# Kernel optimization log

Hardware: AMD Instinct MI355X
Metric: run time of the kernel (lower is better)

The kernel has to match this reference:

```python
import jax, jax.numpy as jnp
import numpy as np

N_NODES = 100000
HIDDEN = 128
N_EDGES = 1000000


def setup_inputs() -> dict:
    key = jax.random.key(0)
    k1, k2, k3 = jax.random.split(key, 3)
    z = jax.random.normal(k1, (N_NODES, HIDDEN), dtype=jnp.float32)
    edge_index = jax.random.randint(k2, (2, N_EDGES), 0, N_NODES, dtype=jnp.int64)
    # xavier_uniform for square matrix: bound = sqrt(6/(fan_in+fan_out))
    bound = float(np.sqrt(6.0 / (HIDDEN + HIDDEN)))
    weights = jax.random.uniform(k3, (HIDDEN, HIDDEN), dtype=jnp.float32,
                                 minval=-bound, maxval=bound)
    return {"z": z, "edge_index": edge_index, "weights": weights}


def reference(z, edge_index, weights):
    # symm=True: symmetrize the bilinear form
    W = weights + weights.T                      # [d, d]
    z_src = z[edge_index[0]]                     # [E, d] gather
    z_dst = z[edge_index[1]]                     # [E, d] gather
    # torch: (W @ z_dst.T).T == z_dst @ W.T
    value = jnp.einsum('ed,dk,ek->e', z_src, W, z_dst)  # row-wise bilinear score
    return jax.nn.sigmoid(value)
```

## Files before the change

### kernel.cpp

```cpp
#include <hip/hip_runtime.h>

#define HIDDEN 128
#define LDSW 130

typedef _Float16 f16;
typedef f16 f16x2 __attribute__((ext_vector_type(2)));
typedef f16 f16x4 __attribute__((ext_vector_type(4)));

static __device__ __forceinline__ float fdot2(f16x2 a, f16x2 b, float c) {
    return __builtin_amdgcn_fdot2(a, b, c, false);
}

__global__ __launch_bounds__(256) void prep_w(const float* __restrict__ w,
                                              f16* __restrict__ wsh_t) {
    int idx = blockIdx.x * 256 + threadIdx.x;
    int j = idx >> 7, k = idx & 127;
    wsh_t[idx] = (f16)(w[k * HIDDEN + j] + w[j * HIDDEN + k]);
}

__global__ __launch_bounds__(256) void gemm_u16(const float* __restrict__ z,
                                               const f16* __restrict__ wsh_t,
                                               f16* __restrict__ zh,
                                               f16* __restrict__ uh) {
    __shared__ f16 wlt[HIDDEN * LDSW];
    __shared__ f16 zt[32 * HIDDEN];
    int tid = threadIdx.x;

    {
        const float4* g = (const float4*)wsh_t;
        #pragma unroll
        for (int it = 0; it < 8; ++it) {
            int idx = it * 256 + tid;
            float4 v = g[idx];
            int j = idx >> 4, kc = idx & 15;
            f16x2* dst = (f16x2*)&wlt[j * LDSW + kc * 8];
            const f16x2* s = (const f16x2*)&v;
            dst[0] = s[0]; dst[1] = s[1]; dst[2] = s[2]; dst[3] = s[3];
        }
    }
    int row0 = blockIdx.x * 32;
    {
        const float4* z4 = (const float4*)(z + (size_t)row0 * HIDDEN);
        f16x2* zl = (f16x2*)zt;
        f16x2* zg = (f16x2*)(zh + (size_t)row0 * HIDDEN);
        #pragma unroll
        for (int it = 0; it < 4; ++it) {
            int idx = it * 256 + tid;
            float4 v = z4[idx];
            f16x2 h0 = {(f16)v.x, (f16)v.y};
            f16x2 h1 = {(f16)v.z, (f16)v.w};
            int r = idx >> 5, c4 = idx & 31;
            zl[r * 64 + c4 * 2]     = h0;
            zl[r * 64 + c4 * 2 + 1] = h1;
            zg[idx * 2]     = h0;
            zg[idx * 2 + 1] = h1;
        }
    }
    __syncthreads();

    int wave = tid >> 6, lane = tid & 63;
    float acc0[8], acc1[8];
    #pragma unroll
    for (int r = 0; r < 8; ++r) { acc0[r] = 0.f; acc1[r] = 0.f; }

    const f16x2* wl2 = (const f16x2*)wlt;
    int c0 = lane * 65, c1 = (lane + 64) * 65;

    #pragma unroll 4
    for (int q = 0; q < 32; ++q) {
        f16x2 w00 = wl2[c0 + 2 * q], w01 = wl2[c0 + 2 * q + 1];
        f16x2 w10 = wl2[c1 + 2 * q], w11 = wl2[c1 + 2 * q + 1];
        #pragma unroll
        for (int r = 0; r < 8; ++r) {
            f16x4 zv = *(const f16x4*)&zt[(wave * 8 + r) * HIDDEN + 4 * q];
            f16x2 z0 = {zv.x, zv.y}, z1 = {zv.z, zv.w};
            acc0[r] = fdot2(z1, w01, fdot2(z0, w00, acc0[r]));
            acc1[r] = fdot2(z1, w11, fdot2(z0, w10, acc1[r]));
        }
    }

    f16* ub = uh + (size_t)(row0 + wave * 8) * HIDDEN;
    #pragma unroll
    for (int r = 0; r < 8; ++r) {
        ub[r * HIDDEN + lane]      = (f16)acc0[r];
        ub[r * HIDDEN + lane + 64] = (f16)acc1[r];
    }
}

__global__ __launch_bounds__(256) void edge_score16(const f16* __restrict__ uh,
                                                    const f16* __restrict__ zh,
                                                    const int* __restrict__ eidx,
                                                    float* __restrict__ out, int E) {
    int tid = threadIdx.x;
    int g = tid >> 4, t = tid & 15;
    int e = blockIdx.x * 16 + g;
    if (e >= E) return;
    int src = eidx[e];
    int dst = eidx[E + e];
    const float4* a4 = (const float4*)(uh + (size_t)src * HIDDEN);
    const float4* b4 = (const float4*)(zh + (size_t)dst * HIDDEN);
    float4 av = a4[t], bv = b4[t];
    const f16x2* ap = (const f16x2*)&av;
    const f16x2* bp = (const f16x2*)&bv;
    float s = 0.f;
    #pragma unroll
    for (int i = 0; i < 4; ++i) s = fdot2(ap[i], bp[i], s);
    #pragma unroll
    for (int off = 8; off > 0; off >>= 1) s += __shfl_down(s, off, 16);
    if (t == 0) out[e] = 1.0f / (1.0f + __expf(-s));
}

extern "C" void kernel_launch(void* const* d_in, const int* in_sizes, int n_in,
                              void* d_out, int out_size, void* d_ws, size_t ws_size,
                              hipStream_t stream) {
    const float* z    = (const float*)d_in[0];
    const int*   eidx = (const int*)d_in[1];
    const float* w    = (const float*)d_in[2];
    float* out = (float*)d_out;

    int nrows = in_sizes[0] / HIDDEN;
    int E = out_size;

    f16* wsh_t = (f16*)d_ws;
    f16* zh    = wsh_t + HIDDEN * HIDDEN;
    f16* uh    = zh + (size_t)nrows * HIDDEN;

    prep_w<<<(HIDDEN * HIDDEN) / 256, 256, 0, stream>>>(w, wsh_t);
    gemm_u16<<<nrows / 32, 256, 0, stream>>>(z, wsh_t, zh, uh);
    edge_score16<<<(E + 15) / 16, 256, 0, stream>>>(uh, zh, eidx, out, E);
}
```

Measured before the change: 184.2 us.

## Split z fp16 conversion into its own kernel and register-tile the GEMM

```diff
diff --git a/kernel.cpp b/kernel.cpp
--- a/kernel.cpp
+++ b/kernel.cpp
@@ -1,11 +1,11 @@
 #include <hip/hip_runtime.h>
 
 #define HIDDEN 128
-#define LDSW 130
+#define LDSW 136
 
 typedef _Float16 f16;
 typedef f16 f16x2 __attribute__((ext_vector_type(2)));
-typedef f16 f16x4 __attribute__((ext_vector_type(4)));
+typedef f16 f16x8 __attribute__((ext_vector_type(8)));
 
 static __device__ __forceinline__ float fdot2(f16x2 a, f16x2 b, float c) {
     return __builtin_amdgcn_fdot2(a, b, c, false);
@@ -18,70 +18,70 @@
     wsh_t[idx] = (f16)(w[k * HIDDEN + j] + w[j * HIDDEN + k]);
 }
 
-__global__ __launch_bounds__(256) void gemm_u16(const float* __restrict__ z,
-                                               const f16* __restrict__ wsh_t,
-                                               f16* __restrict__ zh,
-                                               f16* __restrict__ uh) {
+__global__ __launch_bounds__(256) void conv_z(const float* __restrict__ z,
+                                              f16* __restrict__ zh, int n4) {
+    int idx = blockIdx.x * 256 + threadIdx.x;
+    if (idx >= n4) return;
+    float4 v = ((const float4*)z)[idx];
+    f16x2 h0 = {(f16)v.x, (f16)v.y};
+    f16x2 h1 = {(f16)v.z, (f16)v.w};
+    ((f16x2*)zh)[2 * idx]     = h0;
+    ((f16x2*)zh)[2 * idx + 1] = h1;
+}
+
+__global__ __launch_bounds__(256) void gemm_reg(const f16* __restrict__ zh,
+                                                const f16* __restrict__ wsh_t,
+                                                f16* __restrict__ uh, int nrows) {
     __shared__ f16 wlt[HIDDEN * LDSW];
-    __shared__ f16 zt[32 * HIDDEN];
     int tid = threadIdx.x;
-
     {
-        const float4* g = (const float4*)wsh_t;
+        const f16x8* g = (const f16x8*)wsh_t;
         #pragma unroll
         for (int it = 0; it < 8; ++it) {
             int idx = it * 256 + tid;
-            float4 v = g[idx];
             int j = idx >> 4, kc = idx & 15;
-            f16x2* dst = (f16x2*)&wlt[j * LDSW + kc * 8];
-            const f16x2* s = (const f16x2*)&v;
-            dst[0] = s[0]; dst[1] = s[1]; dst[2] = s[2]; dst[3] = s[3];
-        }
-    }
-    int row0 = blockIdx.x * 32;
-    {
-        const float4* z4 = (const float4*)(z + (size_t)row0 * HIDDEN);
-        f16x2* zl = (f16x2*)zt;
-        f16x2* zg = (f16x2*)(zh + (size_t)row0 * HIDDEN);
-        #pragma unroll
-        for (int it = 0; it < 4; ++it) {
-            int idx = it * 256 + tid;
-            float4 v = z4[idx];
-            f16x2 h0 = {(f16)v.x, (f16)v.y};
-            f16x2 h1 = {(f16)v.z, (f16)v.w};
-            int r = idx >> 5, c4 = idx & 31;
-            zl[r * 64 + c4 * 2]     = h0;
-            zl[r * 64 + c4 * 2 + 1] = h1;
-            zg[idx * 2]     = h0;
-            zg[idx * 2 + 1] = h1;
+            *(f16x8*)&wlt[j * LDSW + kc * 8] = g[idx];
         }
     }
     __syncthreads();
 
     int wave = tid >> 6, lane = tid & 63;
-    float acc0[8], acc1[8];
+    int row0 = blockIdx.x * 64 + wave * 16;
+    if (row0 > nrows - 16) row0 = nrows - 16;
+
+    const f16* zb = zh + (size_t)row0 * HIDDEN;
+    const f16* wc0 = &wlt[lane * LDSW];
+    const f16* wc1 = &wlt[(lane + 64) * LDSW];
+
+    float acc0[16], acc1[16];
     #pragma unroll
-    for (int r = 0; r < 8; ++r) { acc0[r] = 0.f; acc1[r] = 0.f; }
+    for (int r = 0; r < 16; ++r) { acc0[r] = 0.f; acc1[r] = 0.f; }
 
-    const f16x2* wl2 = (const f16x2*)wlt;
-    int c0 = lane * 65, c1 = (lane + 64) * 65;
-
-    #pragma unroll 4
-    for (int q = 0; q < 32; ++q) {
-        f16x2 w00 = wl2[c0 + 2 * q], w01 = wl2[c0 + 2 * q + 1];
-        f16x2 w10 = wl2[c1 + 2 * q], w11 = wl2[c1 + 2 * q + 1];
+    for (int kb = 0; kb < 16; ++kb) {
+        f16x8 wa = *(const f16x8*)&wc0[kb * 8];
+        f16x8 wb = *(const f16x8*)&wc1[kb * 8];
+        f16x8 zv[16];
         #pragma unroll
-        for (int r = 0; r < 8; ++r) {
-            f16x4 zv = *(const f16x4*)&zt[(wave * 8 + r) * HIDDEN + 4 * q];
-            f16x2 z0 = {zv.x, zv.y}, z1 = {zv.z, zv.w};
-            acc0[r] = fdot2(z1, w01, fdot2(z0, w00, acc0[r]));
-            acc1[r] = fdot2(z1, w11, fdot2(z0, w10, acc1[r]));
+        for (int r = 0; r < 16; ++r)
+            zv[r] = *(const f16x8*)&zb[r * HIDDEN + kb * 8];
+        const f16x2* wap = (const f16x2*)&wa;
+        const f16x2* wbp = (const f16x2*)&wb;
+        #pragma unroll
+        for (int r = 0; r < 16; ++r) {
+            const f16x2* zp = (const f16x2*)&zv[r];
+            float a0 = acc0[r], a1 = acc1[r];
+            #pragma unroll
+            for (int i = 0; i < 4; ++i) {
+                a0 = fdot2(zp[i], wap[i], a0);
+                a1 = fdot2(zp[i], wbp[i], a1);
+            }
+            acc0[r] = a0; acc1[r] = a1;
         }
     }
 
-    f16* ub = uh + (size_t)(row0 + wave * 8) * HIDDEN;
+    f16* ub = uh + (size_t)row0 * HIDDEN;
     #pragma unroll
-    for (int r = 0; r < 8; ++r) {
+    for (int r = 0; r < 16; ++r) {
         ub[r * HIDDEN + lane]      = (f16)acc0[r];
         ub[r * HIDDEN + lane + 64] = (f16)acc1[r];
     }
@@ -120,12 +120,14 @@
 
     int nrows = in_sizes[0] / HIDDEN;
     int E = out_size;
+    int n4 = nrows * HIDDEN / 4;
 
     f16* wsh_t = (f16*)d_ws;
     f16* zh    = wsh_t + HIDDEN * HIDDEN;
     f16* uh    = zh + (size_t)nrows * HIDDEN;
 
     prep_w<<<(HIDDEN * HIDDEN) / 256, 256, 0, stream>>>(w, wsh_t);
-    gemm_u16<<<nrows / 32, 256, 0, stream>>>(z, wsh_t, zh, uh);
+    conv_z<<<(n4 + 255) / 256, 256, 0, stream>>>(z, zh, n4);
+    gemm_reg<<<(nrows + 63) / 64, 256, 0, stream>>>(zh, wsh_t, uh, nrows);
     edge_score16<<<(E + 15) / 16, 256, 0, stream>>>(uh, zh, eidx, out, E);
 }
```

After: 219.2 us. 1.19x slower.
